# Performance work log

Hardware: AMD Instinct MI355X
Metric: run time of the kernel (lower is better)

The kernel has to match this reference:

```python
import jax, jax.numpy as jnp
import numpy as np

BEAM = 10; MAX_LEN = 32; PAD = 1; BOS = 2; EOS = 3
NEG = jnp.float32(-1e30)


def lstm_cell(x, h, c, Wih, Whh, bih, bhh):
    # PyTorch LSTMCell gate order: i, f, g, o
    gates = x @ Wih.T + bih + h @ Whh.T + bhh
    i, f, g, o = jnp.split(gates, 4, axis=-1)
    c2 = jax.nn.sigmoid(f) * c + jax.nn.sigmoid(i) * jnp.tanh(g)
    h2 = jax.nn.sigmoid(o) * jnp.tanh(c2)
    return h2, c2


def setup_inputs() -> dict:
    key = jax.random.key(0)
    ks = jax.random.split(key, 14)
    G, P, E, H, S = 1000, 50000, 500, 500, 32
    s = lambda k, shape: jax.random.normal(k, shape, jnp.float32) * 0.05
    return {
        "g_seq": jax.random.randint(ks[0], (S, 1), 0, G),
        "enc_emb": s(ks[1], (G, E)),
        "enc_Wih": s(ks[2], (4 * H, E)), "enc_Whh": s(ks[3], (4 * H, H)),
        "enc_bih": s(ks[4], (4 * H,)), "enc_bhh": s(ks[5], (4 * H,)),
        "dec_emb": s(ks[6], (P, E)),
        "dec_Wih": s(ks[7], (4 * H, E)), "dec_Whh": s(ks[8], (4 * H, H)),
        "dec_bih": s(ks[9], (4 * H,)), "dec_bhh": s(ks[10], (4 * H,)),
        "attn_W": s(ks[11], (H, 2 * H)),
        "out_W": s(ks[12], (P, H)),
        "out_b": s(ks[13], (P,)),
    }


def reference(g_seq, enc_emb, enc_Wih, enc_Whh, enc_bih, enc_bhh,
              dec_emb, dec_Wih, dec_Whh, dec_bih, dec_bhh,
              attn_W, out_W, out_b):
    S = g_seq.shape[0]
    H = enc_Whh.shape[1]
    P = out_W.shape[0]

    # ---- encoder: unidirectional LSTMCell over seq, batch = 1 ----
    e_seq = enc_emb[g_seq[:, 0]]  # (S, E)
    def enc_step(carry, e):
        h, c = carry
        h, c = lstm_cell(e[None, :], h, c, enc_Wih, enc_Whh, enc_bih, enc_bhh)
        return (h, c), h[0]
    h0 = jnp.zeros((1, H), jnp.float32)
    (h, c), outs = jax.lax.scan(enc_step, (h0, h0), e_seq)  # outs: (S, H)

    # expand encoder state / context to beam
    context = jnp.broadcast_to(outs[None, :, :], (BEAM, S, H))
    h = jnp.broadcast_to(h, (BEAM, H))
    c = jnp.broadcast_to(c, (BEAM, H))
    scores = jnp.zeros((BEAM,), jnp.float32)
    tokens = jnp.full((BEAM,), PAD, jnp.int32).at[0].set(BOS)
    row0 = (jnp.arange(BEAM)[:, None] == 0)  # first-step mask: only beam 0 valid

    # ---- beam-search decode loop (run full max_len; early-eos break omitted,
    #      see notes: with eos=3 it only changes output when eos tops beam 0) ----
    def dec_step(carry, t):
        h, c, scores, tokens = carry
        e = dec_emb[tokens]                                   # (BEAM, E)
        h2, c2 = lstm_cell(e, h, c, dec_Wih, dec_Whh, dec_bih, dec_bhh)
        # dot attention
        attn = jax.nn.softmax(jnp.einsum('bsh,bh->bs', context, h2), axis=1)
        wctx = jnp.einsum('bs,bsh->bh', attn, context)
        o = jnp.tanh(jnp.concatenate([h2, wctx], axis=1) @ attn_W.T)
        logp = jax.nn.log_softmax(o @ out_W.T + out_b, axis=1)  # (BEAM, P)
        # first step: only beam 0 participates (original uses workd_lk[0])
        beam_lk = jnp.where(t == 0,
                            jnp.where(row0, logp, NEG),
                            logp + scores[:, None])
        best, idx = jax.lax.top_k(beam_lk.reshape(-1), BEAM)
        prev_k = idx // P
        next_y = idx - prev_k * P
        return (h2[prev_k], c2[prev_k], best, next_y), (prev_k, next_y)

    (_, _, scores, _), (prevKs, nextYs) = jax.lax.scan(
        dec_step, (h, c, scores, tokens), jnp.arange(MAX_LEN))

    # ---- hypothesis traceback, vectorized over beams ----
    def tb_step(k, t):
        tok = nextYs[t][k]
        return prevKs[t][k], tok
    _, toks = jax.lax.scan(tb_step, jnp.arange(BEAM), jnp.arange(MAX_LEN - 1, -1, -1))
    hyps = toks[::-1].T  # (BEAM, MAX_LEN)
    return hyps
```

## Files before the change

### kernel.cpp

```cpp
#include <hip/hip_runtime.h>
#include <math.h>

#define BEAM   10
#define MAXLEN 32
#define SLEN   32
#define HD     500
#define ED     500
#define G4     2000
#define PV     50000
#define NEGF   (-1e30f)
#define NEGD   (-1.0e30)

#define NSTRIP 196
#define CPR    (NSTRIP * BEAM)

typedef unsigned long long u64;

#define OFF_X      0
#define OFF_CBUF   64000
#define OFF_GBUF   65000
#define OFF_CTX    69000
#define OFF_DH     85000
#define OFF_DC     90000
#define OFF_DG     95000
#define OFF_H2     115000
#define OFF_C2     120000
#define OFF_O      125000
#define OFF_SCD    135000
#define OFF_TOK    135040
#define OFF_PREVK  135060
#define OFF_NEXTY  135380
#define OFF_PARTF  136000
#define OFF_CANDF  152000
#define OFF_LOG    160000
#define OFF_PARTD  160284
#define OFF_CAND   165604
#define OFF_OWT    660000
#define NEED_T_BYTES ((size_t)(OFF_OWT + (size_t)HD * PV) * 4)

__device__ __forceinline__ float sigf(float x) { return 1.f / (1.f + expf(-x)); }

__device__ __forceinline__ unsigned fkey(float f) {
    unsigned u = __float_as_uint(f);
    return (u & 0x80000000u) ? ~u : (u | 0x80000000u);
}
__device__ __forceinline__ float unfkey(unsigned k) {
    unsigned u = (k & 0x80000000u) ? (k & 0x7fffffffu) : ~k;
    return __uint_as_float(u);
}

__global__ void k_prep_tr(const int* __restrict__ g_seq, const float* __restrict__ enc_emb,
                          const float* __restrict__ Wih, const float* __restrict__ bih,
                          const float* __restrict__ bhh, float* __restrict__ X,
                          float* __restrict__ cbuf0,
                          const float* __restrict__ outW, float* __restrict__ outW4) {
    __shared__ float t_lds[64][65];
    int tid = threadIdx.x;
    if (blockIdx.x < 16000) {
        if (blockIdx.x == 0) {
            for (int j = tid; j < HD; j += 256) cbuf0[j] = 0.f;
        }
        int wv = (blockIdx.x * 256 + tid) >> 6;
        int lane = tid & 63;
        if (wv >= SLEN * G4) return;
        int t = wv / G4, r = wv - t * G4;
        const float* emb = enc_emb + (size_t)g_seq[t] * ED;
        const float* w = Wih + (size_t)r * ED;
        float acc = 0.f;
        for (int ki = 0; ki < 8; ki++) { int k = ki * 64 + lane; if (k < ED) acc += emb[k] * w[k]; }
        for (int o = 32; o; o >>= 1) acc += __shfl_down(acc, o);
        if (lane == 0) X[t * G4 + r] = acc + bih[r] + bhh[r];
    } else {
        int bid2 = blockIdx.x - 16000;
        int pbase = (bid2 % 782) * 64, kbase = (bid2 / 782) * 64;
        for (int e = 0; e < 16; e++) {
            int idx = e * 256 + tid; int pl = idx >> 6, kl = idx & 63;
            int pp = pbase + pl, kk = kbase + kl;
            t_lds[pl][kl] = (pp < PV && kk < HD) ? outW[(size_t)pp * HD + kk] : 0.f;
        }
        __syncthreads();
        for (int e = 0; e < 4; e++) {
            int idx = e * 256 + tid;
            int pl = idx & 63, kb = idx >> 6;
            int pp = pbase + pl;
            int kglob = kbase + kb * 4;
            if (pp < PV && kglob < HD) {
                float4 v;
                v.x = t_lds[pl][kb * 4 + 0];
                v.y = t_lds[pl][kb * 4 + 1];
                v.z = t_lds[pl][kb * 4 + 2];
                v.w = t_lds[pl][kb * 4 + 3];
                *(float4*)(outW4 + ((size_t)(kbase / 4 + kb) * PV + pp) * 4) = v;
            }
        }
    }
}

__global__ void k_enc(const float* __restrict__ Whh, const float* __restrict__ X,
                      float* __restrict__ gbuf, float* __restrict__ cbuf,
                      float* __restrict__ context, float* __restrict__ dec_h,
                      float* __restrict__ dec_c, double* __restrict__ scores,
                      int* __restrict__ tokens, int t) {
    __shared__ float h_lds[HD];
    const float* gprev = gbuf + ((t + 1) & 1) * G4;
    float*       gcur  = gbuf + (t & 1) * G4;
    const float* cprev = cbuf + ((t + 1) & 1) * HD;
    float*       ccur  = cbuf + (t & 1) * HD;
    int tid = threadIdx.x;
    if (t > 0) {
        for (int j = tid; j < HD; j += 256) {
            float gi = gprev[j], gf = gprev[HD + j], gg = gprev[2 * HD + j], go = gprev[3 * HD + j];
            float c = sigf(gf) * cprev[j] + sigf(gi) * tanhf(gg);
            float h = sigf(go) * tanhf(c);
            h_lds[j] = h;
            if (blockIdx.x == 0) {
                ccur[j] = c;
                context[(t - 1) * HD + j] = h;
                if (t == SLEN) {
                    for (int b = 0; b < BEAM; b++) { dec_h[b * HD + j] = h; dec_c[b * HD + j] = c; }
                }
            }
        }
    } else {
        for (int j = tid; j < HD; j += 256) h_lds[j] = 0.f;
    }
    if (t == SLEN && blockIdx.x == 0 && tid == 0) {
        for (int b = 0; b < BEAM; b++) scores[b] = 0.0;
        tokens[0] = 2; for (int b = 1; b < BEAM; b++) tokens[b] = 1;
    }
    __syncthreads();
    if (t < SLEN) {
        int wv = blockIdx.x * 4 + (tid >> 6), lane = tid & 63;
        for (int r = wv; r < G4; r += 1000) {
            const float* w = Whh + (size_t)r * HD;
            float acc = 0.f;
            for (int ki = 0; ki < 8; ki++) { int k = ki * 64 + lane; if (k < HD) acc += h_lds[k] * w[k]; }
            for (int o = 32; o; o >>= 1) acc += __shfl_down(acc, o);
            if (lane == 0) gcur[r] = X[t * G4 + r] + acc;
        }
    }
}

struct MrgSm {
    double lse[BEAM]; double scl[BEAM];
    u64 rc[BEAM * BEAM];
    double gbv[8]; unsigned gbf[8]; unsigned winf;
    int pk[BEAM]; int ny[BEAM]; double val[BEAM];
};

__device__ __forceinline__ void do_merge(MrgSm* M, const double* __restrict__ part,
                                         const u64* __restrict__ cand,
                                         const double* __restrict__ sc_in,
                                         int m, int tid) {
    int wv = tid >> 6, lane = tid & 63;
    if (tid < BEAM) M->scl[tid] = sc_in[tid];
    for (int r = wv; r < BEAM; r += 8) {
        double s = 0.0;
        for (int i = lane; i < NSTRIP; i += 64) s += part[r * NSTRIP + i];
        for (int o = 32; o; o >>= 1) s += __shfl_down(s, o);
        if (lane == 0) M->lse[r] = log(s);
    }
    for (int r = wv; r < BEAM; r += 8) {
        u64 kk[31];
#pragma unroll
        for (int e = 0; e < 31; e++) {
            int i = lane + e * 64;
            kk[e] = (i < CPR) ? cand[(size_t)r * CPR + i] : 0ull;
        }
        for (int round = 0; round < BEAM; ++round) {
            u64 mx = 0ull;
#pragma unroll
            for (int e = 0; e < 31; e++) if (kk[e] > mx) mx = kk[e];
            for (int o = 32; o; o >>= 1) { u64 t2 = __shfl_down(mx, o); if (t2 > mx) mx = t2; }
            u64 win = __shfl(mx, 0);
#pragma unroll
            for (int e = 0; e < 31; e++) if (kk[e] == win) kk[e] = 0ull;
            if (lane == 0) M->rc[r * BEAM + round] = win;
        }
    }
    __syncthreads();
    double cv = -1.0e308; unsigned cf = 0xFFFFFFFFu;
    if (tid < BEAM * BEAM) {
        u64 k0 = M->rc[tid];
        if (k0) {
            int r2 = tid / BEAM;
            float v = unfkey((unsigned)(k0 >> 32));
            unsigned p = ~((unsigned)k0);
            double v2;
            if (m == 0) v2 = (r2 == 0) ? ((double)v - M->lse[0]) : NEGD;
            else        v2 = ((double)v - M->lse[r2]) + M->scl[r2];
            cv = v2; cf = (unsigned)r2 * PV + p;
        }
    }
    for (int round = 0; round < BEAM; ++round) {
        double bv = cv; unsigned bf = cf;
        for (int o = 32; o; o >>= 1) {
            double ov = __shfl_down(bv, o);
            unsigned of = __shfl_down(bf, o);
            if (ov > bv || (ov == bv && of < bf)) { bv = ov; bf = of; }
        }
        if (lane == 0) { M->gbv[wv] = bv; M->gbf[wv] = bf; }
        __syncthreads();
        if (tid == 0) {
            double xv = M->gbv[0]; unsigned xf = M->gbf[0];
            for (int i = 1; i < 8; i++) {
                if (M->gbv[i] > xv || (M->gbv[i] == xv && M->gbf[i] < xf)) { xv = M->gbv[i]; xf = M->gbf[i]; }
            }
            M->winf = xf;
            int pk = (int)(xf / PV);
            int ny = (int)(xf - (unsigned)pk * PV);
            M->pk[round] = pk; M->ny[round] = ny; M->val[round] = xv;
        }
        __syncthreads();
        if (cf == M->winf) { cv = -1.0e308; cf = 0xFFFFFFFFu; }
        __syncthreads();
    }
}

__global__ __launch_bounds__(512) void k_gates_m(
        const float* __restrict__ decEmb, const float* __restrict__ Wih,
        const float* __restrict__ Whh, const float* __restrict__ bih,
        const float* __restrict__ bhh,
        const double* __restrict__ part, const u64* __restrict__ cand,
        const double* __restrict__ sc_in, double* __restrict__ sc_out,
        const float* __restrict__ h2w, const float* __restrict__ c2w,
        float* __restrict__ dc,
        const float* __restrict__ gbuf, const float* __restrict__ cbuf,
        float* __restrict__ ctx,
        int* __restrict__ prevK, int* __restrict__ nextY,
        float* __restrict__ gates, int t) {
    __shared__ float e_lds[BEAM * ED];
    __shared__ float h_lds[BEAM * HD];
    __shared__ MrgSm M;
    int tid = threadIdx.x, bid = blockIdx.x;
    int wv = tid >> 6, lane = tid & 63;

    if (t > 0) {
        int m = t - 1;
        do_merge(&M, part, cand, sc_in, m, tid);
        if (tid < BEAM && bid == 0) {
            sc_out[tid] = M.val[tid];
            prevK[m * BEAM + tid] = M.pk[tid];
            nextY[m * BEAM + tid] = M.ny[tid];
        }
        __syncthreads();
        for (int idx = tid; idx < BEAM * HD; idx += 512) {
            int b = idx / HD, j = idx - b * HD;
            h_lds[idx] = h2w[M.pk[b] * HD + j];
            e_lds[idx] = decEmb[(size_t)M.ny[b] * ED + j];
            if (bid == 0) dc[idx] = c2w[M.pk[b] * HD + j];
        }
    } else {
        const float* gb = gbuf + G4;
        const float* cp = cbuf + HD;
        for (int j = tid; j < HD; j += 512) {
            float gi = gb[j], gf = gb[HD + j], gg = gb[2 * HD + j], go = gb[3 * HD + j];
            float c = sigf(gf) * cp[j] + sigf(gi) * tanhf(gg);
            float h = sigf(go) * tanhf(c);
            if (bid == 0) {
                ctx[(SLEN - 1) * HD + j] = h;
                for (int b = 0; b < BEAM; b++) dc[b * HD + j] = c;
            }
            for (int b = 0; b < BEAM; b++) h_lds[b * HD + j] = h;
        }
        for (int idx = tid; idx < BEAM * ED; idx += 512) {
            int b = idx / ED, j = idx - b * ED;
            int tk = (b == 0) ? 2 : 1;
            e_lds[idx] = decEmb[(size_t)tk * ED + j];
        }
    }
    __syncthreads();

    for (int rr = 0; rr < 2; ++rr) {
        int r = bid * 16 + wv * 2 + rr;
        const float* wi = Wih + (size_t)r * ED;
        const float* wh = Whh + (size_t)r * HD;
        float acc[BEAM];
#pragma unroll
        for (int b = 0; b < BEAM; b++) acc[b] = 0.f;
        for (int ki = 0; ki < 8; ki++) {
            int k = ki * 64 + lane;
            if (k < ED) {
                float w = wi[k];
#pragma unroll
                for (int b = 0; b < BEAM; b++) acc[b] += w * e_lds[b * ED + k];
            }
        }
        for (int ki = 0; ki < 8; ki++) {
            int k = ki * 64 + lane;
            if (k < HD) {
                float w = wh[k];
#pragma unroll
                for (int b = 0; b < BEAM; b++) acc[b] += w * h_lds[b * HD + k];
            }
        }
#pragma unroll
        for (int b = 0; b < BEAM; b++) {
            float v = acc[b];
            for (int o = 32; o; o >>= 1) v += __shfl_down(v, o);
            acc[b] = v;
        }
        if (lane == 0) {
            float bb = bih[r] + bhh[r];
#pragma unroll
            for (int b = 0; b < BEAM; b++) gates[b * G4 + r] = acc[b] + bb;
        }
    }
}

__global__ __launch_bounds__(256) void k_attn_oproj(
        const float* __restrict__ gates, const float* __restrict__ c_ws,
        const float* __restrict__ context, const float* __restrict__ attnW,
        float* __restrict__ h2_ws, float* __restrict__ c2_ws, float* __restrict__ o_ws) {
    __shared__ float h2_lds[BEAM * HD];
    __shared__ float wctx_lds[BEAM * HD];
    __shared__ float s_lds[BEAM * SLEN];
    __shared__ float a_lds[BEAM * SLEN];
    int tid = threadIdx.x;
    int wv = tid >> 6, lane = tid & 63;
    for (int idx = tid; idx < BEAM * HD; idx += 256) {
        int b = idx / HD, j = idx - b * HD;
        float gi = gates[b * G4 + j], gf = gates[b * G4 + HD + j];
        float gg = gates[b * G4 + 2 * HD + j], go = gates[b * G4 + 3 * HD + j];
        float c = sigf(gf) * c_ws[idx] + sigf(gi) * tanhf(gg);
        float h2 = sigf(go) * tanhf(c);
        h2_lds[idx] = h2;
        if (blockIdx.x == 0) { c2_ws[idx] = c; h2_ws[idx] = h2; }
    }
    __syncthreads();
    for (int si = 0; si < 8; ++si) {
        int s = wv + 4 * si;
        float acc[BEAM];
#pragma unroll
        for (int b = 0; b < BEAM; b++) acc[b] = 0.f;
        for (int ki = 0; ki < 8; ki++) {
            int k = ki * 64 + lane;
            if (k < HD) {
                float c = context[s * HD + k];
#pragma unroll
                for (int b = 0; b < BEAM; b++) acc[b] += c * h2_lds[b * HD + k];
            }
        }
#pragma unroll
        for (int b = 0; b < BEAM; b++) {
            float v = acc[b];
            for (int o = 32; o; o >>= 1) v += __shfl_down(v, o);
            if (lane == 0) s_lds[b * SLEN + s] = v;
        }
    }
    __syncthreads();
    if (wv == 0) {
        for (int b = 0; b < BEAM; ++b) {
            float v = (lane < SLEN) ? s_lds[b * SLEN + lane] : -INFINITY;
            float m = v;
            for (int o = 32; o; o >>= 1) m = fmaxf(m, __shfl_xor(m, o));
            float e = (lane < SLEN) ? expf(v - m) : 0.f;
            float sum = e;
            for (int o = 32; o; o >>= 1) sum += __shfl_xor(sum, o);
            if (lane < SLEN) a_lds[b * SLEN + lane] = e / sum;
        }
    }
    __syncthreads();
    {
        float w0[BEAM], w1[BEAM];
#pragma unroll
        for (int b = 0; b < BEAM; b++) { w0[b] = 0.f; w1[b] = 0.f; }
        int j0 = tid, j1 = tid + 256;
        for (int s = 0; s < SLEN; ++s) {
            float c0 = (j0 < HD) ? context[s * HD + j0] : 0.f;
            float c1 = (j1 < HD) ? context[s * HD + j1] : 0.f;
#pragma unroll
            for (int b = 0; b < BEAM; b++) {
                float a = a_lds[b * SLEN + s];
                w0[b] += a * c0; w1[b] += a * c1;
            }
        }
#pragma unroll
        for (int b = 0; b < BEAM; b++) {
            if (j0 < HD) wctx_lds[b * HD + j0] = w0[b];
            if (j1 < HD) wctx_lds[b * HD + j1] = w1[b];
        }
    }
    __syncthreads();
    int j = blockIdx.x * 4 + wv;
    const float* w = attnW + (size_t)j * 1000;
    float acc[BEAM];
#pragma unroll
    for (int b = 0; b < BEAM; b++) acc[b] = 0.f;
    for (int ki = 0; ki < 16; ki++) {
        int k = ki * 64 + lane;
        if (k < 1000) {
            float wk = w[k];
#pragma unroll
            for (int b = 0; b < BEAM; b++) {
                float h = (k < HD) ? h2_lds[b * HD + k] : wctx_lds[b * HD + k - HD];
                acc[b] += wk * h;
            }
        }
    }
#pragma unroll
    for (int b = 0; b < BEAM; b++) {
        float v = acc[b];
        for (int o = 32; o; o >>= 1) v += __shfl_down(v, o);
        acc[b] = v;
    }
    if (lane == 0) {
#pragma unroll
        for (int b = 0; b < BEAM; b++) o_ws[b * HD + j] = tanhf(acc[b]);
    }
}

__global__ __launch_bounds__(1024) void k_logits_topk(
        const float* __restrict__ outW4, const float* __restrict__ outB,
        const float* __restrict__ o_ws, u64* __restrict__ cand,
        double* __restrict__ part) {
    __shared__ __align__(16) char sm[61440];
    float4* o4 = (float4*)sm;
    float*  pt = (float*)(sm + 20480);
    int tid = threadIdx.x, bid = blockIdx.x;
    int lane = tid & 63;
    int col = tid & 255, kc = tid >> 8;
    for (int idx = tid; idx < BEAM * 125; idx += 1024) {
        int b = idx / 125, kb = idx - b * 125;
        o4[idx] = *(const float4*)(o_ws + b * HD + kb * 4);
    }
    __syncthreads();
    int p = bid * 256 + col;
    bool valid = (p < PV);
    int pc = valid ? p : (PV - 1);
    {
        float acc[BEAM];
#pragma unroll
        for (int b = 0; b < BEAM; b++) acc[b] = 0.f;
        int kb0 = kc * 32, kb1 = (kc == 3) ? 125 : (kb0 + 32);
        const float4* wp = (const float4*)outW4;
        for (int kb = kb0; kb < kb1; ++kb) {
            float4 w = wp[(size_t)kb * PV + pc];
#pragma unroll
            for (int b = 0; b < BEAM; b++) {
                float4 o = o4[b * 125 + kb];
                acc[b] += w.x * o.x + w.y * o.y + w.z * o.z + w.w * o.w;
            }
        }
#pragma unroll
        for (int b = 0; b < BEAM; b++) pt[(kc * 256 + col) * BEAM + b] = acc[b];
    }
    __syncthreads();
    float lg[BEAM];
    if (tid < 256) {
        float ob = outB[pc];
#pragma unroll
        for (int b = 0; b < BEAM; b++)
            lg[b] = pt[(0 * 256 + tid) * BEAM + b] + pt[(1 * 256 + tid) * BEAM + b]
                  + pt[(2 * 256 + tid) * BEAM + b] + pt[(3 * 256 + tid) * BEAM + b] + ob;
    }
    __syncthreads();
    double* pd = (double*)sm;
    u64*    kl = (u64*)(sm + 20480);
    if (tid < 256) {
#pragma unroll
        for (int b = 0; b < BEAM; b++) {
            pd[b * 256 + tid] = valid ? exp((double)lg[b]) : 0.0;
            kl[b * 256 + tid] = valid ? (((u64)fkey(lg[b]) << 32) | (unsigned)(~(unsigned)p)) : 0ull;
        }
    }
    __syncthreads();
    int wv = tid >> 6;
    if (wv < BEAM) {
        int r = wv;
        double s = pd[r * 256 + lane] + pd[r * 256 + 64 + lane]
                 + pd[r * 256 + 128 + lane] + pd[r * 256 + 192 + lane];
        for (int o = 32; o; o >>= 1) s += __shfl_down(s, o);
        if (lane == 0) part[r * NSTRIP + bid] = s;
        u64 kk[4];
#pragma unroll
        for (int j = 0; j < 4; j++) kk[j] = kl[r * 256 + j * 64 + lane];
        for (int round = 0; round < BEAM; round++) {
            u64 m = kk[0];
            if (kk[1] > m) m = kk[1];
            if (kk[2] > m) m = kk[2];
            if (kk[3] > m) m = kk[3];
            for (int o = 32; o; o >>= 1) {
                u64 t2 = __shfl_down(m, o);
                if (t2 > m) m = t2;
            }
            u64 win = __shfl(m, 0);
#pragma unroll
            for (int j = 0; j < 4; j++) if (kk[j] == win) kk[j] = 0ull;
            if (lane == 0) cand[(size_t)r * CPR + bid * 10 + round] = win;
        }
    }
}

__global__ __launch_bounds__(512) void k_final(
        const double* __restrict__ part, const u64* __restrict__ cand,
        const double* __restrict__ sc_in,
        int* __restrict__ prevK, int* __restrict__ nextY, int* __restrict__ out) {
    __shared__ MrgSm M;
    int tid = threadIdx.x;
    do_merge(&M, part, cand, sc_in, MAXLEN - 1, tid);
    if (tid < BEAM) {
        prevK[(MAXLEN - 1) * BEAM + tid] = M.pk[tid];
        nextY[(MAXLEN - 1) * BEAM + tid] = M.ny[tid];
    }
    __syncthreads();
    if (tid < BEAM) {
        int cur = tid;
        for (int tt = MAXLEN - 1; tt >= 0; tt--) {
            out[tid * MAXLEN + tt] = nextY[tt * BEAM + cur];
            cur = prevK[tt * BEAM + cur];
        }
    }
}

__global__ __launch_bounds__(1024) void k_gates(
        const float* __restrict__ dec_emb, const float* __restrict__ Wih,
        const float* __restrict__ Whh, const float* __restrict__ bih,
        const float* __restrict__ bhh, const int* __restrict__ tokens,
        const float* __restrict__ h_ws, float* __restrict__ gates) {
    __shared__ float e_lds[BEAM * ED];
    __shared__ float h_lds[BEAM * HD];
    int tid = threadIdx.x;
    for (int idx = tid; idx < BEAM * ED; idx += 1024) {
        int b = idx / ED, k = idx - b * ED;
        e_lds[idx] = dec_emb[(size_t)tokens[b] * ED + k];
        h_lds[idx] = h_ws[idx];
    }
    __syncthreads();
    int wv = tid >> 6, lane = tid & 63;
    int r = blockIdx.x * 16 + wv;
    const float* wi = Wih + (size_t)r * ED;
    const float* wh = Whh + (size_t)r * HD;
    float acc[BEAM];
#pragma unroll
    for (int b = 0; b < BEAM; b++) acc[b] = 0.f;
    for (int ki = 0; ki < 8; ki++) {
        int k = ki * 64 + lane;
        if (k < ED) {
            float w = wi[k];
#pragma unroll
            for (int b = 0; b < BEAM; b++) acc[b] += w * e_lds[b * ED + k];
        }
    }
    for (int ki = 0; ki < 8; ki++) {
        int k = ki * 64 + lane;
        if (k < HD) {
            float w = wh[k];
#pragma unroll
            for (int b = 0; b < BEAM; b++) acc[b] += w * h_lds[b * HD + k];
        }
    }
#pragma unroll
    for (int b = 0; b < BEAM; b++) {
        float v = acc[b];
        for (int o = 32; o; o >>= 1) v += __shfl_down(v, o);
        acc[b] = v;
    }
    if (lane == 0) {
        float bb = bih[r] + bhh[r];
#pragma unroll
        for (int b = 0; b < BEAM; b++) gates[b * G4 + r] = acc[b] + bb;
    }
}

__global__ void k_logits_f(const float* __restrict__ outW, const float* __restrict__ outB,
                           const float* __restrict__ o_ws, float* __restrict__ logits,
                           double* __restrict__ partials) {
    __shared__ float o_lds[BEAM * HD];
    __shared__ double ered[4][BEAM];
    int tid = threadIdx.x;
    for (int idx = tid; idx < BEAM * HD; idx += 256) o_lds[idx] = o_ws[idx];
    __syncthreads();
    int wv = tid >> 6, lane = tid & 63;
    int w = blockIdx.x * 4 + wv;
    double esum = 0.0;
    for (int pi = 0; pi < 16; pi++) {
        int p = w * 16 + pi;
        if (p >= PV) break;
        const float* wr = outW + (size_t)p * HD;
        float acc[BEAM];
#pragma unroll
        for (int b = 0; b < BEAM; b++) acc[b] = 0.f;
        for (int ki = 0; ki < 8; ki++) {
            int k = ki * 64 + lane;
            if (k < HD) {
                float x = wr[k];
#pragma unroll
                for (int b = 0; b < BEAM; b++) acc[b] += x * o_lds[b * HD + k];
            }
        }
#pragma unroll
        for (int b = 0; b < BEAM; b++)
            for (int o = 32; o; o >>= 1) acc[b] += __shfl_xor(acc[b], o);
        if (lane < BEAM) {
            float lg = 0.f;
#pragma unroll
            for (int b = 0; b < BEAM; b++) if (lane == b) lg = acc[b];
            lg += outB[p];
            logits[(size_t)lane * PV + p] = lg;
            esum += exp((double)lg);
        }
    }
    if (lane < BEAM) ered[wv][lane] = esum;
    __syncthreads();
    if (tid < BEAM) partials[blockIdx.x * BEAM + tid] =
        ered[0][tid] + ered[1][tid] + ered[2][tid] + ered[3][tid];
}

__global__ __launch_bounds__(256) void k_topk_row(const float* __restrict__ logits,
                                                  u64* __restrict__ cands) {
    const int CH = 1563;
    int r = blockIdx.x >> 5, ci = blockIdx.x & 31;
    int base = ci * CH;
    int tid = threadIdx.x;
    int wv = tid >> 6, lane = tid & 63;
    u64 key[7];
#pragma unroll
    for (int e = 0; e < 7; e++) {
        int p = base + e * 256 + tid;
        key[e] = 0ull;
        if (p < base + CH && p < PV) {
            float v = logits[(size_t)r * PV + p];
            key[e] = ((u64)fkey(v) << 32) | (unsigned)(~(unsigned)p);
        }
    }
    __shared__ u64 wred[4];
    __shared__ u64 winlds;
    for (int round = 0; round < BEAM; round++) {
        u64 mx = 0ull;
#pragma unroll
        for (int e = 0; e < 7; e++) if (key[e] > mx) mx = key[e];
        for (int o = 32; o; o >>= 1) {
            u64 other = __shfl_down(mx, o);
            if (other > mx) mx = other;
        }
        if (lane == 0) wred[wv] = mx;
        __syncthreads();
        if (tid == 0) {
            u64 wn = wred[0];
            for (int i = 1; i < 4; i++) if (wred[i] > wn) wn = wred[i];
            winlds = wn;
            cands[blockIdx.x * BEAM + round] = wn;
        }
        __syncthreads();
        u64 win = winlds;
#pragma unroll
        for (int e = 0; e < 7; e++) if (key[e] == win) key[e] = 0ull;
    }
}

__global__ __launch_bounds__(256) void k_merge(
        const double* __restrict__ partials, int npart,
        const u64* __restrict__ cands,
        double* __restrict__ scores, int* __restrict__ tokens,
        const float* __restrict__ h2_ws, const float* __restrict__ c2_ws,
        float* __restrict__ h_ws, float* __restrict__ c_ws,
        int* __restrict__ prevKs, int* __restrict__ nextYs, int t) {
    __shared__ double wredd[4];
    __shared__ double lse_lds[BEAM];
    __shared__ double sc_lds[BEAM];
    __shared__ double bwv[4];
    __shared__ unsigned bwf[4];
    __shared__ unsigned winf_s;
    __shared__ int pk_lds[BEAM];
    __shared__ int ny_lds[BEAM];
    __shared__ double val_lds[BEAM];
    int tid = threadIdx.x;
    int wv = tid >> 6, lane = tid & 63;
    if (tid < BEAM) sc_lds[tid] = scores[tid];
    for (int b = 0; b < BEAM; b++) {
        double s = 0.0;
        for (int j = tid; j < npart; j += 256) s += partials[j * BEAM + b];
        for (int o = 32; o; o >>= 1) s += __shfl_down(s, o);
        if (lane == 0) wredd[wv] = s;
        __syncthreads();
        if (tid == 0) lse_lds[b] = log(wredd[0] + wredd[1] + wredd[2] + wredd[3]);
        __syncthreads();
    }
    double   cv[13];
    unsigned cf[13];
#pragma unroll
    for (int e = 0; e < 13; e++) {
        int c = e * 256 + tid;
        cv[e] = -1.0e308; cf[e] = 0xFFFFFFFFu;
        if (c < 3200) {
            u64 k0 = cands[c];
            if (k0) {
                int r = c / 320;
                float v = unfkey((unsigned)(k0 >> 32));
                unsigned p = ~((unsigned)k0);
                double v2;
                if (t == 0) v2 = (r == 0) ? ((double)v - lse_lds[0]) : (double)NEGF;
                else        v2 = ((double)v - lse_lds[r]) + sc_lds[r];
                cv[e] = v2;
                cf[e] = (unsigned)r * PV + p;
            }
        }
    }
    for (int round = 0; round < BEAM; round++) {
        double bv = -1.0e308; unsigned bf = 0xFFFFFFFFu;
#pragma unroll
        for (int e = 0; e < 13; e++) {
            if (cv[e] > bv || (cv[e] == bv && cf[e] < bf)) { bv = cv[e]; bf = cf[e]; }
        }
        for (int o = 32; o; o >>= 1) {
            double ov = __shfl_down(bv, o);
            unsigned of = __shfl_down(bf, o);
            if (ov > bv || (ov == bv && of < bf)) { bv = ov; bf = of; }
        }
        if (lane == 0) { bwv[wv] = bv; bwf[wv] = bf; }
        __syncthreads();
        if (tid == 0) {
            double xv = bwv[0]; unsigned xf = bwf[0];
            for (int i = 1; i < 4; i++) {
                if (bwv[i] > xv || (bwv[i] == xv && bwf[i] < xf)) { xv = bwv[i]; xf = bwf[i]; }
            }
            winf_s = xf;
            int pk = (int)(xf / PV);
            int ny = (int)(xf - (unsigned)pk * PV);
            pk_lds[round] = pk; ny_lds[round] = ny; val_lds[round] = xv;
        }
        __syncthreads();
        unsigned wff = winf_s;
#pragma unroll
        for (int e = 0; e < 13; e++) {
            if (cf[e] == wff) { cv[e] = -1.0e308; cf[e] = 0xFFFFFFFFu; }
        }
    }
    if (tid < BEAM) {
        scores[tid] = val_lds[tid];
        tokens[tid] = ny_lds[tid];
        prevKs[t * BEAM + tid] = pk_lds[tid];
        nextYs[t * BEAM + tid] = ny_lds[tid];
    }
    __syncthreads();
    for (int idx = tid; idx < BEAM * HD; idx += 256) {
        int i = idx / HD, j = idx - i * HD;
        h_ws[idx] = h2_ws[pk_lds[i] * HD + j];
        c_ws[idx] = c2_ws[pk_lds[i] * HD + j];
    }
}

__global__ void k_traceback(const int* __restrict__ prevKs, const int* __restrict__ nextYs,
                            int* __restrict__ out) {
    int k = threadIdx.x;
    if (k >= BEAM) return;
    int cur = k;
    for (int t = MAXLEN - 1; t >= 0; t--) {
        out[k * MAXLEN + t] = nextYs[t * BEAM + cur];
        cur = prevKs[t * BEAM + cur];
    }
}

extern "C" void kernel_launch(void* const* d_in, const int* in_sizes, int n_in,
                              void* d_out, int out_size, void* d_ws, size_t ws_size,
                              hipStream_t stream) {
    const int*   g_seq  = (const int*)  d_in[0];
    const float* encEmb = (const float*)d_in[1];
    const float* encWih = (const float*)d_in[2];
    const float* encWhh = (const float*)d_in[3];
    const float* encBih = (const float*)d_in[4];
    const float* encBhh = (const float*)d_in[5];
    const float* decEmb = (const float*)d_in[6];
    const float* decWih = (const float*)d_in[7];
    const float* decWhh = (const float*)d_in[8];
    const float* decBih = (const float*)d_in[9];
    const float* decBhh = (const float*)d_in[10];
    const float* attnW  = (const float*)d_in[11];
    const float* outW   = (const float*)d_in[12];
    const float* outB   = (const float*)d_in[13];

    float* ws = (float*)d_ws;
    float*  X     = ws + OFF_X;
    float*  cbuf  = ws + OFF_CBUF;
    float*  gbuf  = ws + OFF_GBUF;
    float*  ctx   = ws + OFF_CTX;
    float*  dh    = ws + OFF_DH;
    float*  dc    = ws + OFF_DC;
    float*  dg    = ws + OFF_DG;
    float*  h2    = ws + OFF_H2;
    float*  c2    = ws + OFF_C2;
    float*  o     = ws + OFF_O;
    double* scb   = (double*)(ws + OFF_SCD);
    int*    tok   = (int*)(ws + OFF_TOK);
    int*    prevK = (int*)(ws + OFF_PREVK);
    int*    nextY = (int*)(ws + OFF_NEXTY);
    float*  outW4 = ws + OFF_OWT;

    bool bigws = (ws_size >= NEED_T_BYTES);

    int prep_grid = bigws ? (16000 + 782 * 8) : 16000;
    k_prep_tr<<<prep_grid, 256, 0, stream>>>(g_seq, encEmb, encWih, encBih, encBhh,
                                             X, cbuf, outW, outW4);

    if (bigws) {
        for (int t = 0; t < SLEN; t++)
            k_enc<<<250, 256, 0, stream>>>(encWhh, X, gbuf, cbuf, ctx, dh, dc, scb, tok, t);

        double* part = (double*)(ws + OFF_PARTD);
        u64*    cand = (u64*)(ws + OFF_CAND);
        for (int t = 0; t < MAXLEN; t++) {
            int m = t - 1;
            const double* sin = scb + ((m & 1) ? 10 : 0);
            double*       sout = scb + (((m + 1) & 1) ? 10 : 0);
            if (t == 0) { sin = scb; sout = scb + 10; }
            k_gates_m<<<125, 512, 0, stream>>>(decEmb, decWih, decWhh, decBih, decBhh,
                                               part, cand, sin, sout,
                                               h2, c2, dc, gbuf, cbuf, ctx,
                                               prevK, nextY, dg, t);
            k_attn_oproj<<<125, 256, 0, stream>>>(dg, dc, ctx, attnW, h2, c2, o);
            k_logits_topk<<<NSTRIP, 1024, 0, stream>>>(outW4, outB, o, cand, part);
        }
        int mf = MAXLEN - 1;
        k_final<<<1, 512, 0, stream>>>(part, cand, scb + ((mf & 1) ? 10 : 0),
                                       prevK, nextY, (int*)d_out);
    } else {
        for (int t = 0; t <= SLEN; t++)
            k_enc<<<250, 256, 0, stream>>>(encWhh, X, gbuf, cbuf, ctx, dh, dc, scb, tok, t);
        double* part  = (double*)(ws + OFF_PARTF);
        u64*    cand  = (u64*)(ws + OFF_CANDF);
        float*  logits = ws + OFF_LOG;
        const int npart = 782;
        for (int t = 0; t < MAXLEN; t++) {
            k_gates<<<125, 1024, 0, stream>>>(decEmb, decWih, decWhh, decBih, decBhh, tok, dh, dg);
            k_attn_oproj<<<125, 256, 0, stream>>>(dg, dc, ctx, attnW, h2, c2, o);
            k_logits_f<<<782, 256, 0, stream>>>(outW, outB, o, logits, part);
            k_topk_row<<<320, 256, 0, stream>>>(logits, cand);
            k_merge<<<1, 256, 0, stream>>>(part, npart, cand, scb, tok, h2, c2, dh, dc, prevK, nextY, t);
        }
        k_traceback<<<1, 64, 0, stream>>>(prevK, nextY, (int*)d_out);
    }
}
```

Measured before the change: 3.994 ms.

## Batch encoder input projection over timesteps and shrink logits strips to more blocks

The encoder input-projection prep now stages all 32 embedded tokens in LDS and has each wave reuse one Wih row load across all timesteps, replacing 16000 tiny per-(t,row) blocks with 125 blocks. The fused logits/top-k kernel moves from 196 blocks of 1024 threads (256 columns) to 392 blocks of 512 threads (128 columns), which spreads the 50000-column output projection over more CUs. The merge step processes the doubled candidate list in two halves, keeping 20 candidates per beam. This costs more partial sums and candidates to merge each step, and adds register pressure from the 32-wide accumulators in prep.

Result: slower. 4.839 ms (+21.1%).

```diff
diff --git a/kernel.cpp b/kernel.cpp
--- a/kernel.cpp
+++ b/kernel.cpp
@@ -11,8 +11,9 @@
 #define NEGF   (-1e30f)
 #define NEGD   (-1.0e30)
 
-#define NSTRIP 196
-#define CPR    (NSTRIP * BEAM)
+#define LNB    392
+#define LCOL   128
+#define CPR    (LNB * BEAM)
 
 typedef unsigned long long u64;
 
@@ -34,7 +35,7 @@
 #define OFF_CANDF  152000
 #define OFF_LOG    160000
 #define OFF_PARTD  160284
-#define OFF_CAND   165604
+#define OFF_CAND   168124
 #define OFF_OWT    660000
 #define NEED_T_BYTES ((size_t)(OFF_OWT + (size_t)HD * PV) * 4)
 
@@ -49,38 +50,63 @@
     return __uint_as_float(u);
 }
 
-__global__ void k_prep_tr(const int* __restrict__ g_seq, const float* __restrict__ enc_emb,
-                          const float* __restrict__ Wih, const float* __restrict__ bih,
-                          const float* __restrict__ bhh, float* __restrict__ X,
-                          float* __restrict__ cbuf0,
-                          const float* __restrict__ outW, float* __restrict__ outW4) {
-    __shared__ float t_lds[64][65];
+__global__ __launch_bounds__(512) void k_prep_tr(
+        const int* __restrict__ g_seq, const float* __restrict__ enc_emb,
+        const float* __restrict__ Wih, const float* __restrict__ bih,
+        const float* __restrict__ bhh, float* __restrict__ X,
+        float* __restrict__ cbuf0,
+        const float* __restrict__ outW, float* __restrict__ outW4) {
+    __shared__ __align__(16) char sm[64000];
     int tid = threadIdx.x;
-    if (blockIdx.x < 16000) {
+    if (blockIdx.x < 125) {
+        float* e_lds = (float*)sm;
         if (blockIdx.x == 0) {
-            for (int j = tid; j < HD; j += 256) cbuf0[j] = 0.f;
-        }
-        int wv = (blockIdx.x * 256 + tid) >> 6;
-        int lane = tid & 63;
-        if (wv >= SLEN * G4) return;
-        int t = wv / G4, r = wv - t * G4;
-        const float* emb = enc_emb + (size_t)g_seq[t] * ED;
-        const float* w = Wih + (size_t)r * ED;
-        float acc = 0.f;
-        for (int ki = 0; ki < 8; ki++) { int k = ki * 64 + lane; if (k < ED) acc += emb[k] * w[k]; }
-        for (int o = 32; o; o >>= 1) acc += __shfl_down(acc, o);
-        if (lane == 0) X[t * G4 + r] = acc + bih[r] + bhh[r];
+            for (int j = tid; j < HD; j += 512) cbuf0[j] = 0.f;
+        }
+        for (int idx = tid; idx < SLEN * ED; idx += 512) {
+            int t = idx / ED, j = idx - t * ED;
+            e_lds[idx] = enc_emb[(size_t)g_seq[t] * ED + j];
+        }
+        __syncthreads();
+        int wv = tid >> 6, lane = tid & 63;
+        for (int rr = 0; rr < 2; ++rr) {
+            int r = blockIdx.x * 16 + wv * 2 + rr;
+            const float* w = Wih + (size_t)r * ED;
+            float acc[SLEN];
+#pragma unroll
+            for (int t = 0; t < SLEN; t++) acc[t] = 0.f;
+            for (int ki = 0; ki < 8; ki++) {
+                int k = ki * 64 + lane;
+                if (k < ED) {
+                    float wk = w[k];
+#pragma unroll
+                    for (int t = 0; t < SLEN; t++) acc[t] += wk * e_lds[t * ED + k];
+                }
+            }
+#pragma unroll
+            for (int t = 0; t < SLEN; t++) {
+                float v = acc[t];
+                for (int o = 32; o; o >>= 1) v += __shfl_down(v, o);
+                acc[t] = v;
+            }
+            if (lane == 0) {
+                float bb = bih[r] + bhh[r];
+#pragma unroll
+                for (int t = 0; t < SLEN; t++) X[t * G4 + r] = acc[t] + bb;
+            }
+        }
     } else {
-        int bid2 = blockIdx.x - 16000;
+        float (*t_lds)[65] = (float(*)[65])sm;
+        int bid2 = blockIdx.x - 125;
         int pbase = (bid2 % 782) * 64, kbase = (bid2 / 782) * 64;
-        for (int e = 0; e < 16; e++) {
-            int idx = e * 256 + tid; int pl = idx >> 6, kl = idx & 63;
+        for (int e = 0; e < 8; e++) {
+            int idx = e * 512 + tid; int pl = idx >> 6, kl = idx & 63;
             int pp = pbase + pl, kk = kbase + kl;
             t_lds[pl][kl] = (pp < PV && kk < HD) ? outW[(size_t)pp * HD + kk] : 0.f;
         }
         __syncthreads();
-        for (int e = 0; e < 4; e++) {
-            int idx = e * 256 + tid;
+        for (int e = 0; e < 2; e++) {
+            int idx = e * 512 + tid;
             int pl = idx & 63, kb = idx >> 6;
             int pp = pbase + pl;
             int kglob = kbase + kb * 4;
@@ -143,7 +169,7 @@
 
 struct MrgSm {
     double lse[BEAM]; double scl[BEAM];
-    u64 rc[BEAM * BEAM];
+    u64 rc[BEAM * 20];
     double gbv[8]; unsigned gbf[8]; unsigned winf;
     int pk[BEAM]; int ny[BEAM]; double val[BEAM];
 };
@@ -156,34 +182,36 @@
     if (tid < BEAM) M->scl[tid] = sc_in[tid];
     for (int r = wv; r < BEAM; r += 8) {
         double s = 0.0;
-        for (int i = lane; i < NSTRIP; i += 64) s += part[r * NSTRIP + i];
+        for (int i = lane; i < LNB; i += 64) s += part[r * LNB + i];
         for (int o = 32; o; o >>= 1) s += __shfl_down(s, o);
         if (lane == 0) M->lse[r] = log(s);
     }
     for (int r = wv; r < BEAM; r += 8) {
-        u64 kk[31];
-#pragma unroll
-        for (int e = 0; e < 31; e++) {
-            int i = lane + e * 64;
-            kk[e] = (i < CPR) ? cand[(size_t)r * CPR + i] : 0ull;
-        }
-        for (int round = 0; round < BEAM; ++round) {
-            u64 mx = 0ull;
-#pragma unroll
-            for (int e = 0; e < 31; e++) if (kk[e] > mx) mx = kk[e];
-            for (int o = 32; o; o >>= 1) { u64 t2 = __shfl_down(mx, o); if (t2 > mx) mx = t2; }
-            u64 win = __shfl(mx, 0);
-#pragma unroll
-            for (int e = 0; e < 31; e++) if (kk[e] == win) kk[e] = 0ull;
-            if (lane == 0) M->rc[r * BEAM + round] = win;
+        for (int half = 0; half < 2; ++half) {
+            u64 kk[31];
+#pragma unroll
+            for (int e = 0; e < 31; e++) {
+                int i = lane + e * 64;
+                kk[e] = (i < 1960) ? cand[(size_t)r * CPR + half * 1960 + i] : 0ull;
+            }
+            for (int round = 0; round < BEAM; ++round) {
+                u64 mx = 0ull;
+#pragma unroll
+                for (int e = 0; e < 31; e++) if (kk[e] > mx) mx = kk[e];
+                for (int o = 32; o; o >>= 1) { u64 t2 = __shfl_down(mx, o); if (t2 > mx) mx = t2; }
+                u64 win = __shfl(mx, 0);
+#pragma unroll
+                for (int e = 0; e < 31; e++) if (kk[e] == win) kk[e] = 0ull;
+                if (lane == 0) M->rc[r * 20 + half * 10 + round] = win;
+            }
         }
     }
     __syncthreads();
     double cv = -1.0e308; unsigned cf = 0xFFFFFFFFu;
-    if (tid < BEAM * BEAM) {
+    if (tid < BEAM * 20) {
         u64 k0 = M->rc[tid];
         if (k0) {
-            int r2 = tid / BEAM;
+            int r2 = tid / 20;
             float v = unfkey((unsigned)(k0 >> 32));
             unsigned p = ~((unsigned)k0);
             double v2;
@@ -410,22 +438,22 @@
     }
 }
 
-__global__ __launch_bounds__(1024) void k_logits_topk(
+__global__ __launch_bounds__(512) void k_logits_topk(
         const float* __restrict__ outW4, const float* __restrict__ outB,
         const float* __restrict__ o_ws, u64* __restrict__ cand,
         double* __restrict__ part) {
-    __shared__ __align__(16) char sm[61440];
+    __shared__ __align__(16) char sm[40960];
     float4* o4 = (float4*)sm;
     float*  pt = (float*)(sm + 20480);
     int tid = threadIdx.x, bid = blockIdx.x;
     int lane = tid & 63;
-    int col = tid & 255, kc = tid >> 8;
-    for (int idx = tid; idx < BEAM * 125; idx += 1024) {
+    int col = tid & 127, kc = tid >> 7;
+    for (int idx = tid; idx < BEAM * 125; idx += 512) {
         int b = idx / 125, kb = idx - b * 125;
         o4[idx] = *(const float4*)(o_ws + b * HD + kb * 4);
     }
     __syncthreads();
-    int p = bid * 256 + col;
+    int p = bid * LCOL + col;
     bool valid = (p < PV);
     int pc = valid ? p : (PV - 1);
     {
@@ -443,50 +471,46 @@
             }
         }
 #pragma unroll
-        for (int b = 0; b < BEAM; b++) pt[(kc * 256 + col) * BEAM + b] = acc[b];
+        for (int b = 0; b < BEAM; b++) pt[(kc * LCOL + col) * BEAM + b] = acc[b];
     }
     __syncthreads();
     float lg[BEAM];
-    if (tid < 256) {
+    if (tid < LCOL) {
         float ob = outB[pc];
 #pragma unroll
         for (int b = 0; b < BEAM; b++)
-            lg[b] = pt[(0 * 256 + tid) * BEAM + b] + pt[(1 * 256 + tid) * BEAM + b]
-                  + pt[(2 * 256 + tid) * BEAM + b] + pt[(3 * 256 + tid) * BEAM + b] + ob;
+            lg[b] = pt[(0 * LCOL + tid) * BEAM + b] + pt[(1 * LCOL + tid) * BEAM + b]
+                  + pt[(2 * LCOL + tid) * BEAM + b] + pt[(3 * LCOL + tid) * BEAM + b] + ob;
     }
     __syncthreads();
     double* pd = (double*)sm;
-    u64*    kl = (u64*)(sm + 20480);
-    if (tid < 256) {
+    u64*    kl = (u64*)(sm + 10240);
+    if (tid < LCOL) {
 #pragma unroll
         for (int b = 0; b < BEAM; b++) {
-            pd[b * 256 + tid] = valid ? exp((double)lg[b]) : 0.0;
-            kl[b * 256 + tid] = valid ? (((u64)fkey(lg[b]) << 32) | (unsigned)(~(unsigned)p)) : 0ull;
+            pd[b * LCOL + tid] = valid ? exp((double)lg[b]) : 0.0;
+            kl[b * LCOL + tid] = valid ? (((u64)fkey(lg[b]) << 32) | (unsigned)(~(unsigned)p)) : 0ull;
         }
     }
     __syncthreads();
     int wv = tid >> 6;
-    if (wv < BEAM) {
-        int r = wv;
-        double s = pd[r * 256 + lane] + pd[r * 256 + 64 + lane]
-                 + pd[r * 256 + 128 + lane] + pd[r * 256 + 192 + lane];
+    for (int r = wv; r < BEAM; r += 8) {
+        double s = pd[r * LCOL + lane] + pd[r * LCOL + 64 + lane];
         for (int o = 32; o; o >>= 1) s += __shfl_down(s, o);
-        if (lane == 0) part[r * NSTRIP + bid] = s;
-        u64 kk[4];
-#pragma unroll
-        for (int j = 0; j < 4; j++) kk[j] = kl[r * 256 + j * 64 + lane];
+        if (lane == 0) part[r * LNB + bid] = s;
+        u64 kk[2];
+        kk[0] = kl[r * LCOL + lane];
+        kk[1] = kl[r * LCOL + 64 + lane];
         for (int round = 0; round < BEAM; round++) {
             u64 m = kk[0];
             if (kk[1] > m) m = kk[1];
-            if (kk[2] > m) m = kk[2];
-            if (kk[3] > m) m = kk[3];
             for (int o = 32; o; o >>= 1) {
                 u64 t2 = __shfl_down(m, o);
                 if (t2 > m) m = t2;
             }
             u64 win = __shfl(m, 0);
-#pragma unroll
-            for (int j = 0; j < 4; j++) if (kk[j] == win) kk[j] = 0ull;
+            if (kk[0] == win) kk[0] = 0ull;
+            if (kk[1] == win) kk[1] = 0ull;
             if (lane == 0) cand[(size_t)r * CPR + bid * 10 + round] = win;
         }
     }
@@ -789,8 +813,8 @@
 
     bool bigws = (ws_size >= NEED_T_BYTES);
 
-    int prep_grid = bigws ? (16000 + 782 * 8) : 16000;
-    k_prep_tr<<<prep_grid, 256, 0, stream>>>(g_seq, encEmb, encWih, encBih, encBhh,
+    int prep_grid = bigws ? (125 + 782 * 8) : 125;
+    k_prep_tr<<<prep_grid, 512, 0, stream>>>(g_seq, encEmb, encWih, encBih, encBhh,
                                              X, cbuf, outW, outW4);
 
     if (bigws) {
@@ -809,7 +833,7 @@
                                                h2, c2, dc, gbuf, cbuf, ctx,
                                                prevK, nextY, dg, t);
             k_attn_oproj<<<125, 256, 0, stream>>>(dg, dc, ctx, attnW, h2, c2, o);
-            k_logits_topk<<<NSTRIP, 1024, 0, stream>>>(outW4, outB, o, cand, part);
+            k_logits_topk<<<LNB, 512, 0, stream>>>(outW4, outB, o, cand, part);
         }
         int mf = MAXLEN - 1;
         k_final<<<1, 512, 0, stream>>>(part, cand, scb + ((mf & 1) ? 10 : 0),
```
